# Performance work log

Hardware: AMD Instinct MI355X
Metric: run time of the kernel (lower is better)

The kernel has to match this reference:

```python
import jax, jax.numpy as jnp
import numpy as np

DIM = 768
HEADS = 12
HEAD_DIM = DIM // HEADS
SCALE = HEAD_DIM ** -0.5


def setup_inputs() -> dict:
    key = jax.random.key(0)
    ks = jax.random.split(key, 6)
    B, N = 4, 2048
    x = jax.random.normal(ks[0], (B, N, DIM), dtype=jnp.float32)
    s = DIM ** -0.5
    Wq = jax.random.normal(ks[1], (DIM, DIM), dtype=jnp.float32) * s
    Wk = jax.random.normal(ks[2], (DIM, DIM), dtype=jnp.float32) * s
    Wv = jax.random.normal(ks[3], (DIM, DIM), dtype=jnp.float32) * s
    Wp = jax.random.normal(ks[4], (DIM, DIM), dtype=jnp.float32) * s
    bp = jnp.zeros((DIM,), dtype=jnp.float32)
    return {"x": x, "Wq": Wq, "Wk": Wk, "Wv": Wv, "Wp": Wp, "bp": bp}


def reference(x, Wq, Wk, Wv, Wp, bp):
    B, N, C = x.shape
    # separate Q/K/V linears (no bias, qkv_bias=False); torch Linear: x @ W.T
    q = (x @ Wq.T).reshape(B, N, HEADS, HEAD_DIM).transpose(0, 2, 1, 3)
    k = (x @ Wk.T).reshape(B, N, HEADS, HEAD_DIM).transpose(0, 2, 1, 3)
    v = (x @ Wv.T).reshape(B, N, HEADS, HEAD_DIM).transpose(0, 2, 1, 3)
    # explicit full [B,H,N,N] attention matrix, as in the source
    attn = jnp.einsum("bhqd,bhkd->bhqk", q, k) * SCALE
    attn = jax.nn.softmax(attn, axis=-1)
    out = jnp.einsum("bhqk,bhkd->bhqd", attn, v)
    out = out.transpose(0, 2, 1, 3).reshape(B, N, C)
    return out @ Wp.T + bp
```

## Files before the change

### kernel.cpp

```cpp
#include <hip/hip_runtime.h>
#include <cstdint>

#define DIM   768
#define HEADS 12
#define HDIM  64
#define BATCH 4
#define SEQ   2048
#define MROWS (BATCH*SEQ)

typedef __bf16 bf16;
typedef __bf16 bf16x4_t __attribute__((ext_vector_type(4)));
typedef __bf16 bf16x8_t __attribute__((ext_vector_type(8)));
typedef float  f32x4_t  __attribute__((ext_vector_type(4)));
typedef float  f32x16_t __attribute__((ext_vector_type(16)));

__global__ void cast_bf16_kernel(const float* __restrict__ src, bf16* __restrict__ dst, int n4) {
    int i = blockIdx.x * blockDim.x + threadIdx.x;
    if (i >= n4) return;
    const float4 v = reinterpret_cast<const float4*>(src)[i];
    bf16x4_t o;
    o[0] = (bf16)v.x; o[1] = (bf16)v.y; o[2] = (bf16)v.z; o[3] = (bf16)v.w;
    reinterpret_cast<bf16x4_t*>(dst)[i] = o;
}

__global__ void cast_w4_kernel(const float* __restrict__ s0, const float* __restrict__ s1,
                               const float* __restrict__ s2, const float* __restrict__ s3,
                               bf16* __restrict__ d0, bf16* __restrict__ d1,
                               bf16* __restrict__ d2, bf16* __restrict__ d3, int n4) {
    int i = blockIdx.x * blockDim.x + threadIdx.x;
    if (i >= n4) return;
    int y = blockIdx.y;
    const float* src = (y == 0) ? s0 : (y == 1) ? s1 : (y == 2) ? s2 : s3;
    bf16* dst        = (y == 0) ? d0 : (y == 1) ? d1 : (y == 2) ? d2 : d3;
    const float4 v = reinterpret_cast<const float4*>(src)[i];
    bf16x4_t o;
    o[0] = (bf16)v.x; o[1] = (bf16)v.y; o[2] = (bf16)v.z; o[3] = (bf16)v.w;
    reinterpret_cast<bf16x4_t*>(dst)[i] = o;
}

__device__ __forceinline__ void gload_lds16(const bf16* g, bf16* l) {
    __builtin_amdgcn_global_load_lds((const __attribute__((address_space(1))) void*)g,
                                     (__attribute__((address_space(3))) void*)l, 16, 0, 0);
}

__device__ __forceinline__ int swz4(int row) { return (row & 3) ^ ((row >> 2) & 3); }

__global__ __launch_bounds__(256, 3) void qkvv_gemm(
        const bf16* __restrict__ X,
        const bf16* __restrict__ Wq, const bf16* __restrict__ Wk, const bf16* __restrict__ Wv,
        bf16* __restrict__ Q, bf16* __restrict__ Kd, bf16* __restrict__ Vt)
{
    __shared__ __align__(16) bf16 SM[2][2][128 * 32];
    const int tid  = threadIdx.x;

    const int d  = blockIdx.x + 6 * blockIdx.y + 384 * blockIdx.z;
    const int L  = (d & 7) * 144 + (d >> 3);
    const int z  = L / 384;
    const int rem = L % 384;
    const int m0 = (rem % 6) * 128;
    const int n0 = (rem / 6) * 128;

    const bf16* Ap = (z == 0) ? Wq : (z == 1 ? Wk : Wv);
    const int lane = tid & 63;
    const int w    = tid >> 6;
    const int wm   = (w & 1) * 64, wn = (w >> 1) * 64;
    const int lr   = lane & 15, quad = lane >> 4;

    const int sr1 = tid >> 2, sc1 = tid & 3;
    const int sr2 = (tid + 256) >> 2;
    const int g1 = sc1 ^ swz4(sr1);
    const int g2 = sc1 ^ swz4(sr2);

    f32x4_t acc[4][4] = {};

    {
        gload_lds16(Ap + (size_t)(m0 + sr1) * DIM + g1 * 8, &SM[0][0][tid * 8]);
        gload_lds16(X  + (size_t)(n0 + sr1) * DIM + g1 * 8, &SM[0][1][tid * 8]);
        gload_lds16(Ap + (size_t)(m0 + sr2) * DIM + g2 * 8, &SM[0][0][(tid + 256) * 8]);
        gload_lds16(X  + (size_t)(n0 + sr2) * DIM + g2 * 8, &SM[0][1][(tid + 256) * 8]);
    }
    __syncthreads();

    int buf = 0;
    for (int p = 0; p < DIM / 32; ++p) {
        if (p + 1 < DIM / 32) {
            int kk = (p + 1) * 32;
            gload_lds16(Ap + (size_t)(m0 + sr1) * DIM + kk + g1 * 8, &SM[buf ^ 1][0][tid * 8]);
            gload_lds16(X  + (size_t)(n0 + sr1) * DIM + kk + g1 * 8, &SM[buf ^ 1][1][tid * 8]);
            gload_lds16(Ap + (size_t)(m0 + sr2) * DIM + kk + g2 * 8, &SM[buf ^ 1][0][(tid + 256) * 8]);
            gload_lds16(X  + (size_t)(n0 + sr2) * DIM + kk + g2 * 8, &SM[buf ^ 1][1][(tid + 256) * 8]);
        }
        bf16x8_t af[4], bfr[4];
        #pragma unroll
        for (int i = 0; i < 4; ++i) {
            int row = wm + i * 16 + lr;
            af[i] = *reinterpret_cast<const bf16x8_t*>(&SM[buf][0][row * 32 + (quad ^ swz4(row)) * 8]);
        }
        #pragma unroll
        for (int j = 0; j < 4; ++j) {
            int row = wn + j * 16 + lr;
            bfr[j] = *reinterpret_cast<const bf16x8_t*>(&SM[buf][1][row * 32 + (quad ^ swz4(row)) * 8]);
        }
        #pragma unroll
        for (int i = 0; i < 4; ++i)
            #pragma unroll
            for (int j = 0; j < 4; ++j)
                acc[i][j] = __builtin_amdgcn_mfma_f32_16x16x32_bf16(af[i], bfr[j], acc[i][j], 0, 0, 0);
        __syncthreads();
        buf ^= 1;
    }

    if (z == 2) {
        bf16* CT = &SM[0][0][0];
        #pragma unroll
        for (int i = 0; i < 4; ++i) {
            int ml = wm + i * 16 + quad * 4;
            #pragma unroll
            for (int j = 0; j < 4; ++j) {
                int p   = lr >> 2;
                int pp  = ((p & 1) << 1) | (p >> 1);
                int nl  = wn + j * 16 + (pp << 2) + (lr & 3);
                #pragma unroll
                for (int r = 0; r < 4; ++r)
                    CT[(ml + r) * 128 + nl] = (bf16)acc[i][j][r];
            }
        }
        __syncthreads();
        const int rr = tid >> 4, cc = tid & 15;
        #pragma unroll
        for (int rnd = 0; rnd < 8; ++rnd) {
            int ml = rnd * 16 + rr;
            *reinterpret_cast<bf16x8_t*>(&Vt[(size_t)(m0 + ml) * MROWS + n0 + cc * 8]) =
                *reinterpret_cast<const bf16x8_t*>(&CT[ml * 128 + cc * 8]);
        }
    } else {
        const float sc = (z == 0) ? 0.18033688011112042f : 1.0f;
        bf16* dst = (z == 0) ? Q : Kd;
        #pragma unroll
        for (int i = 0; i < 4; ++i) {
            int mb = m0 + wm + i * 16 + quad * 4;
            int h  = mb >> 6, d0 = mb & 63;
            #pragma unroll
            for (int j = 0; j < 4; ++j) {
                int sample = n0 + wn + j * 16 + lr;
                int b = sample >> 11, srow = sample & 2047;
                bf16x4_t o;
                #pragma unroll
                for (int r = 0; r < 4; ++r)
                    o[r] = (bf16)(acc[i][j][r] * sc);
                *reinterpret_cast<bf16x4_t*>(
                    &dst[(((size_t)b * HEADS + h) * SEQ + srow) * HDIM + d0]) = o;
            }
        }
    }
}

__global__ __launch_bounds__(256, 4) void out_gemm(
        const bf16* __restrict__ A,
        const bf16* __restrict__ W,
        const float* __restrict__ bias,
        float* __restrict__ out)
{
    __shared__ __align__(16) bf16 SA[2][64 * 32];
    __shared__ __align__(16) bf16 SB[2][128 * 32];
    const int tid  = threadIdx.x;

    const int d  = blockIdx.x + 6 * blockIdx.y;
    const int L  = (d & 7) * 96 + (d >> 3);
    const int n0 = (L % 6) * 128;
    const int m0 = (L / 6) * 64;

    const int lane = tid & 63;
    const int w    = tid >> 6;
    const int wm   = (w & 1) * 32, wn = (w >> 1) * 64;
    const int lr   = lane & 15, quad = lane >> 4;

    const int sr1 = tid >> 2, sc1 = tid & 3;
    const int sr2 = (tid + 256) >> 2;
    const int g1 = sc1 ^ swz4(sr1);
    const int g2 = sc1 ^ swz4(sr2);

    f32x4_t acc[2][4] = {};

    {
        gload_lds16(A + (size_t)(m0 + sr1) * DIM + g1 * 8, &SA[0][tid * 8]);
        gload_lds16(W + (size_t)(n0 + sr1) * DIM + g1 * 8, &SB[0][tid * 8]);
        gload_lds16(W + (size_t)(n0 + sr2) * DIM + g2 * 8, &SB[0][(tid + 256) * 8]);
    }
    __syncthreads();

    int buf = 0;
    for (int p = 0; p < DIM / 32; ++p) {
        if (p + 1 < DIM / 32) {
            int kk = (p + 1) * 32;
            gload_lds16(A + (size_t)(m0 + sr1) * DIM + kk + g1 * 8, &SA[buf ^ 1][tid * 8]);
            gload_lds16(W + (size_t)(n0 + sr1) * DIM + kk + g1 * 8, &SB[buf ^ 1][tid * 8]);
            gload_lds16(W + (size_t)(n0 + sr2) * DIM + kk + g2 * 8, &SB[buf ^ 1][(tid + 256) * 8]);
        }
        bf16x8_t af[2], bfr[4];
        #pragma unroll
        for (int i = 0; i < 2; ++i) {
            int row = wm + i * 16 + lr;
            af[i] = *reinterpret_cast<const bf16x8_t*>(&SA[buf][row * 32 + (quad ^ swz4(row)) * 8]);
        }
        #pragma unroll
        for (int j = 0; j < 4; ++j) {
            int row = wn + j * 16 + lr;
            bfr[j] = *reinterpret_cast<const bf16x8_t*>(&SB[buf][row * 32 + (quad ^ swz4(row)) * 8]);
        }
        #pragma unroll
        for (int i = 0; i < 2; ++i)
            #pragma unroll
            for (int j = 0; j < 4; ++j)
                acc[i][j] = __builtin_amdgcn_mfma_f32_16x16x32_bf16(af[i], bfr[j], acc[i][j], 0, 0, 0);
        __syncthreads();
        buf ^= 1;
    }

    #pragma unroll
    for (int i = 0; i < 2; ++i) {
        int mbase = m0 + wm + i * 16 + quad * 4;
        #pragma unroll
        for (int j = 0; j < 4; ++j) {
            int n = n0 + wn + j * 16 + lr;
            float bv = bias[n];
            #pragma unroll
            for (int r = 0; r < 4; ++r) {
                int m = mbase + r;
                out[(size_t)m * DIM + n] = acc[i][j][r] + bv;
            }
        }
    }
}

__global__ __launch_bounds__(256, 3) void attn_kernel(
        const bf16* __restrict__ Q, const bf16* __restrict__ Kd,
        const bf16* __restrict__ Vt, bf16* __restrict__ Ab)
{
    __shared__ __align__(16) bf16 SH[5 * 64 * 64];
    bf16* Kb = SH;
    bf16* Vb = SH + 2 * 4096;

    const int tid  = threadIdx.x;

    const int dd = blockIdx.x + 16 * blockIdx.y;
    const int L  = (dd & 7) * 96 + (dd >> 3);
    const int bh = L >> 4;
    const int q0 = (L & 15) * 128;

    const int b    = bh / HEADS, h = bh % HEADS;
    const int lane = tid & 63, w = tid >> 6;
    const int l31  = lane & 31, hw = lane >> 5;
    const int wq   = w * 32;

    const size_t qkbase = (size_t)bh * SEQ * HDIM;
    const size_t vbase  = (size_t)h * HDIM * MROWS + (size_t)b * SEQ;

    const int src_row  = tid >> 3, src_ch = tid & 7;
    const int src_gch  = src_ch ^ (src_row & 7);
    const int src_row2 = (tid + 256) >> 3;
    const int src_gch2 = src_ch ^ (src_row2 & 7);
    const int loff1 = src_row  * 64 + src_ch * 8;
    const int loff2 = src_row2 * 64 + src_ch * 8;

    {
        bf16* Qst = Vb + 4096;
        #pragma unroll
        for (int i = 0; i < 4; ++i) {
            int c = tid + i * 256;
            int row = c >> 3, ch = c & 7;
            int gch = ch ^ (row & 7);
            gload_lds16(Q + qkbase + (size_t)(q0 + row) * HDIM + gch * 8, Qst + row * 64 + ch * 8);
        }
    }

    const bf16* kp1 = Kd + qkbase + (size_t)src_row  * HDIM + src_gch  * 8;
    const bf16* kp2 = Kd + qkbase + (size_t)src_row2 * HDIM + src_gch2 * 8;
    const bf16* vp1 = Vt + vbase  + (size_t)src_row  * MROWS + src_gch  * 8;
    const bf16* vp2 = Vt + vbase  + (size_t)src_row2 * MROWS + src_gch2 * 8;
    const ptrdiff_t kstep = 64 * HDIM, vstep = 64;

    gload_lds16(kp1, Kb + loff1); gload_lds16(kp2, Kb + loff2);
    gload_lds16(vp1, Vb + loff1); gload_lds16(vp2, Vb + loff2);
    __syncthreads();

    bf16x8_t qf[4];
    {
        const bf16* Qst = Vb + 4096;
        int row = wq + l31;
        #pragma unroll
        for (int g = 0; g < 4; ++g) {
            int ch = (2 * g + hw) ^ (row & 7);
            qf[g] = *reinterpret_cast<const bf16x8_t*>(&Qst[row * 64 + ch * 8]);
        }
    }
    __syncthreads();

    f32x16_t oacc[2] = {};
    f32x16_t rsacc  = {};
    bf16x8_t pk[4];
    bf16x8_t ones8;
    #pragma unroll
    for (int i = 0; i < 8; ++i) ones8[i] = (bf16)1.0f;

    int vprev = 2, vcur = 0, vnext = 1;

    for (int it = 0; it < SEQ / 64; ++it) {
        if (it + 1 < SEQ / 64) {
            const ptrdiff_t g = (ptrdiff_t)(it + 1);
            bf16* kd = Kb + ((it + 1) & 1) * 4096;
            bf16* vd = Vb + vnext * 4096;
            gload_lds16(kp1 + g * kstep, kd + loff1); gload_lds16(kp2 + g * kstep, kd + loff2);
            gload_lds16(vp1 + g * vstep, vd + loff1); gload_lds16(vp2 + g * vstep, vd + loff2);
        }

        const bf16* Ks = Kb + (it & 1) * 4096;

        f32x16_t sacc[2] = {};
        __builtin_amdgcn_s_setprio(1);
        #pragma unroll
        for (int kc = 0; kc < 2; ++kc) {
            int row = kc * 32 + l31;
            #pragma unroll
            for (int g = 0; g < 4; ++g) {
                int ch = (2 * g + hw) ^ (row & 7);
                bf16x8_t af = *reinterpret_cast<const bf16x8_t*>(&Ks[row * 64 + ch * 8]);
                sacc[kc] = __builtin_amdgcn_mfma_f32_32x32x16_bf16(af, qf[g], sacc[kc], 0, 0, 0);
            }
        }

        if (it > 0) {
            const bf16* Vs = Vb + vprev * 4096;
            #pragma unroll
            for (int dc = 0; dc < 2; ++dc) {
                int row = dc * 32 + l31;
                #pragma unroll
                for (int kg = 0; kg < 4; ++kg) {
                    int myc = (2 * kg + hw) ^ (row & 7);
                    bf16x8_t bb = *reinterpret_cast<const bf16x8_t*>(&Vs[row * 64 + myc * 8]);
                    oacc[dc] = __builtin_amdgcn_mfma_f32_32x32x16_bf16(pk[kg], bb, oacc[dc], 0, 0, 0);
                }
            }
            #pragma unroll
            for (int kg = 0; kg < 4; ++kg)
                rsacc = __builtin_amdgcn_mfma_f32_32x32x16_bf16(pk[kg], ones8, rsacc, 0, 0, 0);
        }
        __builtin_amdgcn_s_setprio(0);

        #pragma unroll
        for (int kg = 0; kg < 4; ++kg) {
            #pragma unroll
            for (int j = 0; j < 8; ++j)
                pk[kg][j] = (bf16)__builtin_amdgcn_exp2f(sacc[kg >> 1][(kg & 1) * 8 + j]);
        }

        __syncthreads();
        int tmp = vprev; vprev = vcur; vcur = vnext; vnext = tmp;
    }

    {
        const bf16* Vs = Vb + vprev * 4096;
        #pragma unroll
        for (int dc = 0; dc < 2; ++dc) {
            int row = dc * 32 + l31;
            #pragma unroll
            for (int kg = 0; kg < 4; ++kg) {
                int myc = (2 * kg + hw) ^ (row & 7);
                bf16x8_t bb = *reinterpret_cast<const bf16x8_t*>(&Vs[row * 64 + myc * 8]);
                oacc[dc] = __builtin_amdgcn_mfma_f32_32x32x16_bf16(pk[kg], bb, oacc[dc], 0, 0, 0);
            }
        }
        #pragma unroll
        for (int kg = 0; kg < 4; ++kg)
            rsacc = __builtin_amdgcn_mfma_f32_32x32x16_bf16(pk[kg], ones8, rsacc, 0, 0, 0);
    }

    float inv[16];
    #pragma unroll
    for (int r = 0; r < 16; ++r)
        inv[r] = 1.0f / rsacc[r];
    #pragma unroll
    for (int dc = 0; dc < 2; ++dc) {
        int d = dc * 32 + l31;
        #pragma unroll
        for (int r = 0; r < 16; ++r) {
            int q = q0 + wq + (r & 3) + 8 * (r >> 2) + 4 * hw;
            Ab[((size_t)b * SEQ + q) * DIM + h * HDIM + d] = (bf16)(oacc[dc][r] * inv[r]);
        }
    }
}

extern "C" void kernel_launch(void* const* d_in, const int* in_sizes, int n_in,
                              void* d_out, int out_size, void* d_ws, size_t ws_size,
                              hipStream_t stream) {
    (void)in_sizes; (void)n_in; (void)out_size; (void)ws_size;
    const float* x  = (const float*)d_in[0];
    const float* Wq = (const float*)d_in[1];
    const float* Wk = (const float*)d_in[2];
    const float* Wv = (const float*)d_in[3];
    const float* Wp = (const float*)d_in[4];
    const float* bp = (const float*)d_in[5];
    float* out = (float*)d_out;

    char* ws = (char*)d_ws;
    size_t off = 0;
    auto alloc = [&](size_t bytes) {
        void* p = ws + off;
        off += (bytes + 255) & ~(size_t)255;
        return p;
    };
    const size_t big = (size_t)MROWS * DIM * sizeof(bf16);
    const size_t wsz = (size_t)DIM * DIM * sizeof(bf16);
    bf16* Xb  = (bf16*)alloc(big);
    bf16* Qb  = (bf16*)alloc(big);
    bf16* Kb  = (bf16*)alloc(big);
    bf16* Vtb = (bf16*)alloc(big);
    bf16* Wqb = (bf16*)alloc(wsz);
    bf16* Wkb = (bf16*)alloc(wsz);
    bf16* Wvb = (bf16*)alloc(wsz);
    bf16* Wpb = (bf16*)alloc(wsz);
    bf16* Ab  = Xb;

    const int x4 = MROWS * DIM / 4;
    cast_bf16_kernel<<<(x4 + 255) / 256, 256, 0, stream>>>(x, Xb, x4);
    const int w4 = DIM * DIM / 4;
    cast_w4_kernel<<<dim3((w4 + 255) / 256, 4), 256, 0, stream>>>(
        Wq, Wk, Wv, Wp, Wqb, Wkb, Wvb, Wpb, w4);

    qkvv_gemm<<<dim3(DIM / 128, MROWS / 128, 3), 256, 0, stream>>>(
        Xb, Wqb, Wkb, Wvb, Qb, Kb, Vtb);

    attn_kernel<<<dim3(SEQ / 128, BATCH * HEADS), 256, 0, stream>>>(Qb, Kb, Vtb, Ab);

    out_gemm<<<dim3(DIM / 128, MROWS / 64), 256, 0, stream>>>(Ab, Wpb, bp, out);
}
```

Before: 217.0 us.

## Load K fragments directly from global into registers instead of staging in LDS

K tiles are no longer copied into shared memory. Each lane now reads its MFMA A-operand fragments straight from global memory into registers, prefetching the next tile right after the QK^T MFMAs. This drops the K double buffer, shrinking LDS from 5 to 3 tiles, and removes the LDS read traffic for K. In exchange, every block issues uncoalesced 16-byte global loads and carries more registers, and global load latency may now be exposed within the iteration.

```diff
diff --git a/kernel.cpp b/kernel.cpp
--- a/kernel.cpp
+++ b/kernel.cpp
@@ -237,9 +237,8 @@
         const bf16* __restrict__ Q, const bf16* __restrict__ Kd,
         const bf16* __restrict__ Vt, bf16* __restrict__ Ab)
 {
-    __shared__ __align__(16) bf16 SH[5 * 64 * 64];
-    bf16* Kb = SH;
-    bf16* Vb = SH + 2 * 4096;
+    __shared__ __align__(16) bf16 SH[3 * 64 * 64];
+    bf16* Vb = SH;
 
     const int tid  = threadIdx.x;
 
@@ -274,13 +273,10 @@
         }
     }
 
-    const bf16* kp1 = Kd + qkbase + (size_t)src_row  * HDIM + src_gch  * 8;
-    const bf16* kp2 = Kd + qkbase + (size_t)src_row2 * HDIM + src_gch2 * 8;
-    const bf16* vp1 = Vt + vbase  + (size_t)src_row  * MROWS + src_gch  * 8;
-    const bf16* vp2 = Vt + vbase  + (size_t)src_row2 * MROWS + src_gch2 * 8;
-    const ptrdiff_t kstep = 64 * HDIM, vstep = 64;
-
-    gload_lds16(kp1, Kb + loff1); gload_lds16(kp2, Kb + loff2);
+    const bf16* vp1 = Vt + vbase + (size_t)src_row  * MROWS + src_gch  * 8;
+    const bf16* vp2 = Vt + vbase + (size_t)src_row2 * MROWS + src_gch2 * 8;
+    const ptrdiff_t vstep = 64;
+
     gload_lds16(vp1, Vb + loff1); gload_lds16(vp2, Vb + loff2);
     __syncthreads();
 
@@ -295,6 +291,15 @@
         }
     }
     __syncthreads();
+
+    const bf16* kl = Kd + qkbase + (size_t)l31 * HDIM + hw * 8;
+
+    bf16x8_t kf[2][4];
+    #pragma unroll
+    for (int kc = 0; kc < 2; ++kc)
+        #pragma unroll
+        for (int g = 0; g < 4; ++g)
+            kf[kc][g] = *reinterpret_cast<const bf16x8_t*>(kl + kc * 2048 + g * 16);
 
     f32x16_t oacc[2] = {};
     f32x16_t rsacc  = {};
@@ -304,33 +309,37 @@
     for (int i = 0; i < 8; ++i) ones8[i] = (bf16)1.0f;
 
     int vprev = 2, vcur = 0, vnext = 1;
-
-    for (int it = 0; it < SEQ / 64; ++it) {
-        if (it + 1 < SEQ / 64) {
+    const int NT = SEQ / 64;
+
+    for (int it = 0; it < NT; ++it) {
+        if (it + 1 < NT) {
             const ptrdiff_t g = (ptrdiff_t)(it + 1);
-            bf16* kd = Kb + ((it + 1) & 1) * 4096;
             bf16* vd = Vb + vnext * 4096;
-            gload_lds16(kp1 + g * kstep, kd + loff1); gload_lds16(kp2 + g * kstep, kd + loff2);
-            gload_lds16(vp1 + g * vstep, vd + loff1); gload_lds16(vp2 + g * vstep, vd + loff2);
-        }
-
-        const bf16* Ks = Kb + (it & 1) * 4096;
+            gload_lds16(vp1 + g * vstep, vd + loff1);
+            gload_lds16(vp2 + g * vstep, vd + loff2);
+        }
 
         f32x16_t sacc[2] = {};
         __builtin_amdgcn_s_setprio(1);
         #pragma unroll
-        for (int kc = 0; kc < 2; ++kc) {
-            int row = kc * 32 + l31;
-            #pragma unroll
-            for (int g = 0; g < 4; ++g) {
-                int ch = (2 * g + hw) ^ (row & 7);
-                bf16x8_t af = *reinterpret_cast<const bf16x8_t*>(&Ks[row * 64 + ch * 8]);
-                sacc[kc] = __builtin_amdgcn_mfma_f32_32x32x16_bf16(af, qf[g], sacc[kc], 0, 0, 0);
-            }
+        for (int kc = 0; kc < 2; ++kc)
+            #pragma unroll
+            for (int g = 0; g < 4; ++g)
+                sacc[kc] = __builtin_amdgcn_mfma_f32_32x32x16_bf16(kf[kc][g], qf[g], sacc[kc], 0, 0, 0);
+        __builtin_amdgcn_s_setprio(0);
+
+        if (it + 1 < NT) {
+            const bf16* kn = kl + (size_t)(it + 1) * 4096;
+            #pragma unroll
+            for (int kc = 0; kc < 2; ++kc)
+                #pragma unroll
+                for (int g = 0; g < 4; ++g)
+                    kf[kc][g] = *reinterpret_cast<const bf16x8_t*>(kn + kc * 2048 + g * 16);
         }
 
         if (it > 0) {
             const bf16* Vs = Vb + vprev * 4096;
+            __builtin_amdgcn_s_setprio(1);
             #pragma unroll
             for (int dc = 0; dc < 2; ++dc) {
                 int row = dc * 32 + l31;
@@ -344,8 +353,8 @@
             #pragma unroll
             for (int kg = 0; kg < 4; ++kg)
                 rsacc = __builtin_amdgcn_mfma_f32_32x32x16_bf16(pk[kg], ones8, rsacc, 0, 0, 0);
-        }
-        __builtin_amdgcn_s_setprio(0);
+            __builtin_amdgcn_s_setprio(0);
+        }
 
         #pragma unroll
         for (int kg = 0; kg < 4; ++kg) {
```

Result: slower. 253.1 us (+16.6%).

## Process 64 query rows per wave with 128-thread attention blocks

Applied to the files above, without the earlier changes.

Attention blocks drop from 4 waves to 2, and each wave now handles two 32-row query groups. Every K and V fragment read from LDS therefore feeds two MFMAs, halving LDS reads per flop. The PV and row-sum MFMAs are also moved ahead of the QK^T MFMAs in each iteration to change the overlap with exp. The cost is roughly double the accumulator registers per wave and only 2 waves per block (launch bounds 128,1), which lowers occupancy and latency hiding.

```diff
diff --git a/kernel.cpp b/kernel.cpp
--- a/kernel.cpp
+++ b/kernel.cpp
@@ -233,7 +233,7 @@
     }
 }
 
-__global__ __launch_bounds__(256, 3) void attn_kernel(
+__global__ __launch_bounds__(128, 1) void attn_kernel(
         const bf16* __restrict__ Q, const bf16* __restrict__ Kd,
         const bf16* __restrict__ Vt, bf16* __restrict__ Ab)
 {
@@ -251,86 +251,82 @@
     const int b    = bh / HEADS, h = bh % HEADS;
     const int lane = tid & 63, w = tid >> 6;
     const int l31  = lane & 31, hw = lane >> 5;
-    const int wq   = w * 32;
+    const int wq   = w * 64;
 
     const size_t qkbase = (size_t)bh * SEQ * HDIM;
     const size_t vbase  = (size_t)h * HDIM * MROWS + (size_t)b * SEQ;
 
-    const int src_row  = tid >> 3, src_ch = tid & 7;
-    const int src_gch  = src_ch ^ (src_row & 7);
-    const int src_row2 = (tid + 256) >> 3;
-    const int src_gch2 = src_ch ^ (src_row2 & 7);
-    const int loff1 = src_row  * 64 + src_ch * 8;
-    const int loff2 = src_row2 * 64 + src_ch * 8;
+    const int sch = tid & 7;
+    int srow[4], loff[4];
+    const bf16 *kp[4], *vp[4];
+    #pragma unroll
+    for (int j = 0; j < 4; ++j) {
+        int c = tid + j * 128;
+        srow[j] = c >> 3;
+        int gch = sch ^ (srow[j] & 7);
+        loff[j] = srow[j] * 64 + sch * 8;
+        kp[j] = Kd + qkbase + (size_t)srow[j] * HDIM  + gch * 8;
+        vp[j] = Vt + vbase  + (size_t)srow[j] * MROWS + gch * 8;
+    }
+    const ptrdiff_t kstep = 64 * HDIM, vstep = 64;
 
     {
         bf16* Qst = Vb + 4096;
         #pragma unroll
-        for (int i = 0; i < 4; ++i) {
-            int c = tid + i * 256;
+        for (int i = 0; i < 8; ++i) {
+            int c = tid + i * 128;
             int row = c >> 3, ch = c & 7;
             int gch = ch ^ (row & 7);
             gload_lds16(Q + qkbase + (size_t)(q0 + row) * HDIM + gch * 8, Qst + row * 64 + ch * 8);
         }
     }
 
-    const bf16* kp1 = Kd + qkbase + (size_t)src_row  * HDIM + src_gch  * 8;
-    const bf16* kp2 = Kd + qkbase + (size_t)src_row2 * HDIM + src_gch2 * 8;
-    const bf16* vp1 = Vt + vbase  + (size_t)src_row  * MROWS + src_gch  * 8;
-    const bf16* vp2 = Vt + vbase  + (size_t)src_row2 * MROWS + src_gch2 * 8;
-    const ptrdiff_t kstep = 64 * HDIM, vstep = 64;
-
-    gload_lds16(kp1, Kb + loff1); gload_lds16(kp2, Kb + loff2);
-    gload_lds16(vp1, Vb + loff1); gload_lds16(vp2, Vb + loff2);
+    #pragma unroll
+    for (int j = 0; j < 4; ++j) {
+        gload_lds16(kp[j], Kb + loff[j]);
+        gload_lds16(vp[j], Vb + loff[j]);
+    }
     __syncthreads();
 
-    bf16x8_t qf[4];
+    bf16x8_t qf[2][4];
     {
         const bf16* Qst = Vb + 4096;
-        int row = wq + l31;
-        #pragma unroll
-        for (int g = 0; g < 4; ++g) {
-            int ch = (2 * g + hw) ^ (row & 7);
-            qf[g] = *reinterpret_cast<const bf16x8_t*>(&Qst[row * 64 + ch * 8]);
+        #pragma unroll
+        for (int qg = 0; qg < 2; ++qg) {
+            int row = wq + qg * 32 + l31;
+            #pragma unroll
+            for (int g = 0; g < 4; ++g) {
+                int ch = (2 * g + hw) ^ (row & 7);
+                qf[qg][g] = *reinterpret_cast<const bf16x8_t*>(&Qst[row * 64 + ch * 8]);
+            }
         }
     }
     __syncthreads();
 
-    f32x16_t oacc[2] = {};
-    f32x16_t rsacc  = {};
-    bf16x8_t pk[4];
+    f32x16_t oacc[2][2] = {};
+    f32x16_t rsacc[2]  = {};
+    bf16x8_t pk[2][4];
     bf16x8_t ones8;
     #pragma unroll
     for (int i = 0; i < 8; ++i) ones8[i] = (bf16)1.0f;
 
     int vprev = 2, vcur = 0, vnext = 1;
-
-    for (int it = 0; it < SEQ / 64; ++it) {
-        if (it + 1 < SEQ / 64) {
-            const ptrdiff_t g = (ptrdiff_t)(it + 1);
+    const int NT = SEQ / 64;
+
+    for (int it = 0; it < NT; ++it) {
+        if (it + 1 < NT) {
             bf16* kd = Kb + ((it + 1) & 1) * 4096;
             bf16* vd = Vb + vnext * 4096;
-            gload_lds16(kp1 + g * kstep, kd + loff1); gload_lds16(kp2 + g * kstep, kd + loff2);
-            gload_lds16(vp1 + g * vstep, vd + loff1); gload_lds16(vp2 + g * vstep, vd + loff2);
-        }
-
-        const bf16* Ks = Kb + (it & 1) * 4096;
-
-        f32x16_t sacc[2] = {};
-        __builtin_amdgcn_s_setprio(1);
-        #pragma unroll
-        for (int kc = 0; kc < 2; ++kc) {
-            int row = kc * 32 + l31;
-            #pragma unroll
-            for (int g = 0; g < 4; ++g) {
-                int ch = (2 * g + hw) ^ (row & 7);
-                bf16x8_t af = *reinterpret_cast<const bf16x8_t*>(&Ks[row * 64 + ch * 8]);
-                sacc[kc] = __builtin_amdgcn_mfma_f32_32x32x16_bf16(af, qf[g], sacc[kc], 0, 0, 0);
+            #pragma unroll
+            for (int j = 0; j < 4; ++j) {
+                gload_lds16(kp[j] + (ptrdiff_t)(it + 1) * kstep, kd + loff[j]);
+                gload_lds16(vp[j] + (ptrdiff_t)(it + 1) * vstep, vd + loff[j]);
             }
         }
 
         if (it > 0) {
             const bf16* Vs = Vb + vprev * 4096;
+            __builtin_amdgcn_s_setprio(1);
             #pragma unroll
             for (int dc = 0; dc < 2; ++dc) {
                 int row = dc * 32 + l31;
@@ -338,21 +334,42 @@
                 for (int kg = 0; kg < 4; ++kg) {
                     int myc = (2 * kg + hw) ^ (row & 7);
                     bf16x8_t bb = *reinterpret_cast<const bf16x8_t*>(&Vs[row * 64 + myc * 8]);
-                    oacc[dc] = __builtin_amdgcn_mfma_f32_32x32x16_bf16(pk[kg], bb, oacc[dc], 0, 0, 0);
+                    oacc[0][dc] = __builtin_amdgcn_mfma_f32_32x32x16_bf16(pk[0][kg], bb, oacc[0][dc], 0, 0, 0);
+                    oacc[1][dc] = __builtin_amdgcn_mfma_f32_32x32x16_bf16(pk[1][kg], bb, oacc[1][dc], 0, 0, 0);
                 }
             }
             #pragma unroll
-            for (int kg = 0; kg < 4; ++kg)
-                rsacc = __builtin_amdgcn_mfma_f32_32x32x16_bf16(pk[kg], ones8, rsacc, 0, 0, 0);
+            for (int kg = 0; kg < 4; ++kg) {
+                rsacc[0] = __builtin_amdgcn_mfma_f32_32x32x16_bf16(pk[0][kg], ones8, rsacc[0], 0, 0, 0);
+                rsacc[1] = __builtin_amdgcn_mfma_f32_32x32x16_bf16(pk[1][kg], ones8, rsacc[1], 0, 0, 0);
+            }
+            __builtin_amdgcn_s_setprio(0);
+        }
+
+        const bf16* Ks = Kb + (it & 1) * 4096;
+        f32x16_t sacc[2][2] = {};
+        __builtin_amdgcn_s_setprio(1);
+        #pragma unroll
+        for (int kc = 0; kc < 2; ++kc) {
+            int row = kc * 32 + l31;
+            #pragma unroll
+            for (int g = 0; g < 4; ++g) {
+                int ch = (2 * g + hw) ^ (row & 7);
+                bf16x8_t af = *reinterpret_cast<const bf16x8_t*>(&Ks[row * 64 + ch * 8]);
+                sacc[0][kc] = __builtin_amdgcn_mfma_f32_32x32x16_bf16(af, qf[0][g], sacc[0][kc], 0, 0, 0);
+                sacc[1][kc] = __builtin_amdgcn_mfma_f32_32x32x16_bf16(af, qf[1][g], sacc[1][kc], 0, 0, 0);
+            }
         }
         __builtin_amdgcn_s_setprio(0);
 
         #pragma unroll
-        for (int kg = 0; kg < 4; ++kg) {
-            #pragma unroll
-            for (int j = 0; j < 8; ++j)
-                pk[kg][j] = (bf16)__builtin_amdgcn_exp2f(sacc[kg >> 1][(kg & 1) * 8 + j]);
-        }
+        for (int qg = 0; qg < 2; ++qg)
+            #pragma unroll
+            for (int kg = 0; kg < 4; ++kg) {
+                #pragma unroll
+                for (int j = 0; j < 8; ++j)
+                    pk[qg][kg][j] = (bf16)__builtin_amdgcn_exp2f(sacc[qg][kg >> 1][(kg & 1) * 8 + j]);
+            }
 
         __syncthreads();
         int tmp = vprev; vprev = vcur; vcur = vnext; vnext = tmp;
@@ -367,25 +384,31 @@
             for (int kg = 0; kg < 4; ++kg) {
                 int myc = (2 * kg + hw) ^ (row & 7);
                 bf16x8_t bb = *reinterpret_cast<const bf16x8_t*>(&Vs[row * 64 + myc * 8]);
-                oacc[dc] = __builtin_amdgcn_mfma_f32_32x32x16_bf16(pk[kg], bb, oacc[dc], 0, 0, 0);
-            }
-        }
-        #pragma unroll
-        for (int kg = 0; kg < 4; ++kg)
-            rsacc = __builtin_amdgcn_mfma_f32_32x32x16_bf16(pk[kg], ones8, rsacc, 0, 0, 0);
-    }
-
-    float inv[16];
+                oacc[0][dc] = __builtin_amdgcn_mfma_f32_32x32x16_bf16(pk[0][kg], bb, oacc[0][dc], 0, 0, 0);
+                oacc[1][dc] = __builtin_amdgcn_mfma_f32_32x32x16_bf16(pk[1][kg], bb, oacc[1][dc], 0, 0, 0);
+            }
+        }
+        #pragma unroll
+        for (int kg = 0; kg < 4; ++kg) {
+            rsacc[0] = __builtin_amdgcn_mfma_f32_32x32x16_bf16(pk[0][kg], ones8, rsacc[0], 0, 0, 0);
+            rsacc[1] = __builtin_amdgcn_mfma_f32_32x32x16_bf16(pk[1][kg], ones8, rsacc[1], 0, 0, 0);
+        }
+    }
+
     #pragma unroll
-    for (int r = 0; r < 16; ++r)
-        inv[r] = 1.0f / rsacc[r];
-    #pragma unroll
-    for (int dc = 0; dc < 2; ++dc) {
-        int d = dc * 32 + l31;
-        #pragma unroll
-        for (int r = 0; r < 16; ++r) {
-            int q = q0 + wq + (r & 3) + 8 * (r >> 2) + 4 * hw;
-            Ab[((size_t)b * SEQ + q) * DIM + h * HDIM + d] = (bf16)(oacc[dc][r] * inv[r]);
+    for (int qg = 0; qg < 2; ++qg) {
+        float inv[16];
+        #pragma unroll
+        for (int r = 0; r < 16; ++r)
+            inv[r] = 1.0f / rsacc[qg][r];
+        #pragma unroll
+        for (int dc = 0; dc < 2; ++dc) {
+            int d = dc * 32 + l31;
+            #pragma unroll
+            for (int r = 0; r < 16; ++r) {
+                int q = q0 + wq + qg * 32 + (r & 3) + 8 * (r >> 2) + 4 * hw;
+                Ab[((size_t)b * SEQ + q) * DIM + h * HDIM + d] = (bf16)(oacc[qg][dc][r] * inv[r]);
+            }
         }
     }
 }
@@ -430,7 +453,7 @@
     qkvv_gemm<<<dim3(DIM / 128, MROWS / 128, 3), 256, 0, stream>>>(
         Xb, Wqb, Wkb, Wvb, Qb, Kb, Vtb);
 
-    attn_kernel<<<dim3(SEQ / 128, BATCH * HEADS), 256, 0, stream>>>(Qb, Kb, Vtb, Ab);
+    attn_kernel<<<dim3(SEQ / 128, BATCH * HEADS), 128, 0, stream>>>(Qb, Kb, Vtb, Ab);
 
     out_gemm<<<dim3(DIM / 128, MROWS / 64), 256, 0, stream>>>(Ab, Wpb, bp, out);
 }
```

Measured after the change: 239.9 us. 10.5% more time.
